# Performance work log

Hardware: AMD Instinct MI355X
Metric: run time of the kernel (lower is better)

Reference implementation:

```python
import jax, jax.numpy as jnp
import numpy as np

EPS = 1e-12  # torch F.normalize eps
NUM_HEADS = 4
DT = 0.25
NUM_STEPS = 4


def _l2norm(x, axis=-1):
    n = jnp.sqrt(jnp.sum(x * x, axis=axis, keepdims=True))
    return x / jnp.maximum(n, EPS)


def setup_inputs() -> dict:
    key = jax.random.key(0)
    k0, k1, k2, k3, k4 = jax.random.split(key, 5)
    B, T, D = 4, 2048, 256
    z = jax.random.normal(k0, (B, T, D), dtype=jnp.float32)
    omega = jax.random.normal(k1, (1, 1, D), dtype=jnp.float32) * 0.1
    Wqk = jax.random.normal(k2, (2 * D, D), dtype=jnp.float32) * (1.0 / np.sqrt(D))
    Wout = jax.random.normal(k3, (D, D), dtype=jnp.float32) * (1.0 / np.sqrt(D))
    bout = jax.random.normal(k4, (D,), dtype=jnp.float32) * 0.01
    return {"z": z, "omega": omega, "Wqk": Wqk, "Wout": Wout, "bout": bout}


def _kuramoto(x, omega, Wqk, Wout, bout):
    # x: [B, T, D]
    B, T, D = x.shape
    hd = D // NUM_HEADS
    qk = x @ Wqk.T  # [B, T, 2D]
    q, k = jnp.split(qk, 2, axis=-1)
    q = _l2norm(q.reshape(B, T, NUM_HEADS, hd))  # cosine-normalized per head
    k = _l2norm(k.reshape(B, T, NUM_HEADS, hd))
    # coupling: [B, H, T, T] cosine similarity
    coupling = jnp.einsum("bqhd,bkhd->bhqk", q, k)
    # sin nonlinearity replaces softmax
    force = jnp.einsum("bhqk,bkhd->bqhd", jnp.sin(coupling), k).reshape(B, T, D)
    return omega + force @ Wout.T + bout


def reference(z, omega, Wqk, Wout, bout):
    def f(x):
        return _kuramoto(x, omega, Wqk, Wout, bout)

    x = z
    for _ in range(NUM_STEPS):
        x = _l2norm(x)
        k1 = f(x)
        k2 = f(x + DT / 2 * k1)
        k3 = f(x + DT / 2 * k2)
        k4 = f(x + DT * k3)
        x = x + DT / 6 * (k1 + 2 * k2 + 2 * k3 + k4)
    return _l2norm(x)
```

## Files before the change

kernel.cpp:

```cpp
#include <hip/hip_runtime.h>
#include <cmath>

#define NB 4
#define TT 2048
#define DD 256
#define NH 4
#define BT (NB*TT)

static constexpr float DT_ = 0.25f;

typedef _Float16 f16x8 __attribute__((ext_vector_type(8)));
typedef _Float16 f16x4 __attribute__((ext_vector_type(4)));
typedef float    f32x4 __attribute__((ext_vector_type(4)));

static constexpr size_t HSZ = (size_t)NB * NH * TT * 64;
static constexpr size_t FSZ = (size_t)BT * 256;

__global__ __launch_bounds__(256)
void split_weights(const float* __restrict__ Wqk, const float* __restrict__ Wout,
                   _Float16* __restrict__ WqkH, _Float16* __restrict__ WqkL,
                   _Float16* __restrict__ WoutH, _Float16* __restrict__ WoutL)
{
    const int idx = blockIdx.x * 256 + threadIdx.x;
    const float4 v = (idx < 32768) ? ((const float4*)Wqk)[idx]
                                   : ((const float4*)Wout)[idx - 32768];
    f16x4 h, l;
    h[0]=(_Float16)v.x; l[0]=(_Float16)(v.x-(float)h[0]);
    h[1]=(_Float16)v.y; l[1]=(_Float16)(v.y-(float)h[1]);
    h[2]=(_Float16)v.z; l[2]=(_Float16)(v.z-(float)h[2]);
    h[3]=(_Float16)v.w; l[3]=(_Float16)(v.w-(float)h[3]);
    if (idx < 32768) { ((f16x4*)WqkH)[idx] = h; ((f16x4*)WqkL)[idx] = l; }
    else { ((f16x4*)WoutH)[idx-32768] = h; ((f16x4*)WoutL)[idx-32768] = l; }
}

__global__ __launch_bounds__(256)
void comb_weights(const float* __restrict__ Wqk, const float* __restrict__ Wout,
                  const float* __restrict__ omega, const float* __restrict__ bout,
                  _Float16* __restrict__ WcombH, _Float16* __restrict__ WcombL,
                  float* __restrict__ qkob)
{
    __shared__ float qrow[256];
    __shared__ float pr[256];
    const int n = blockIdx.x;
    const int k = threadIdx.x;
    qrow[k] = Wqk[n * 256 + k];
    __syncthreads();
    float s = 0.f;
    for (int m = 0; m < 256; ++m) s = fmaf(qrow[m], Wout[m * 256 + k], s);
    const _Float16 h = (_Float16)s;
    WcombH[n * 256 + k] = h;
    WcombL[n * 256 + k] = (_Float16)(s - (float)h);
    pr[k] = (omega[k] + bout[k]) * qrow[k];
    __syncthreads();
    if (k == 0) {
        float t = 0.f;
        for (int i = 0; i < 256; ++i) t += pr[i];
        qkob[n] = t;
    }
}

__global__ __launch_bounds__(256)
void l2norm_rows(const float* __restrict__ src, float* __restrict__ dst,
                 _Float16* __restrict__ dstH, _Float16* __restrict__ dstL) {
    const int wave = threadIdx.x >> 6;
    const int lane = threadIdx.x & 63;
    const size_t row = (size_t)blockIdx.x * 4 + wave;
    float4 v = ((const float4*)(src + row * DD))[lane];
    float ss = v.x*v.x + v.y*v.y + v.z*v.z + v.w*v.w;
    #pragma unroll
    for (int off = 32; off; off >>= 1) ss += __shfl_xor(ss, off, 64);
    const float inv = 1.0f / fmaxf(sqrtf(ss), 1e-12f);
    v.x *= inv; v.y *= inv; v.z *= inv; v.w *= inv;
    ((float4*)(dst + row * DD))[lane] = v;
    if (dstH != nullptr) {
        f16x4 h, l;
        h[0]=(_Float16)v.x; l[0]=(_Float16)(v.x-(float)h[0]);
        h[1]=(_Float16)v.y; l[1]=(_Float16)(v.y-(float)h[1]);
        h[2]=(_Float16)v.z; l[2]=(_Float16)(v.z-(float)h[2]);
        h[3]=(_Float16)v.w; l[3]=(_Float16)(v.w-(float)h[3]);
        ((f16x4*)(dstH + row * DD))[lane] = h;
        ((f16x4*)(dstL + row * DD))[lane] = l;
    }
}

__global__ __launch_bounds__(256)
void gemm_mfma(const _Float16* __restrict__ AH, const _Float16* __restrict__ AL,
               const float* __restrict__ Fp, float* __restrict__ Facc,
               const _Float16* __restrict__ BH, const _Float16* __restrict__ BL,
               float* __restrict__ qkx, const float* __restrict__ qkob,
               const float* __restrict__ omega, const float* __restrict__ bout,
               const float* __restrict__ xin, float* __restrict__ xout,
               _Float16* __restrict__ Qhi, _Float16* __restrict__ Qlo,
               _Float16* __restrict__ Khi, _Float16* __restrict__ Klo,
               _Float16* __restrict__ KtrH,
               int mode, float cc, int faccm)
{
    __shared__ _Float16 Ah[128 * 72];
    __shared__ _Float16 Al[128 * 72];
    __shared__ _Float16 Bh[64 * 72];
    __shared__ _Float16 Bl[64 * 72];
    const int m0 = blockIdx.x * 128, n0 = blockIdx.y * 64;
    const int t  = threadIdx.x;
    const int w  = t >> 6;
    const int l  = t & 63;
    const int lr = l & 15;
    const int lq = l >> 4;

    f32x4 acc[2][4];
    #pragma unroll
    for (int s = 0; s < 2; ++s)
        #pragma unroll
        for (int nt = 0; nt < 4; ++nt) acc[s][nt] = (f32x4){0.f,0.f,0.f,0.f};

    for (int kc = 0; kc < 4; ++kc) {
        const int k0 = kc * 64;
        __syncthreads();
        if (mode == 0) {
            #pragma unroll
            for (int s2 = 0; s2 < 4; ++s2) {
                const int idx = t + 256 * s2;
                const int r = idx >> 3, c8 = (idx & 7) * 8;
                *(uint4*)&Ah[r * 72 + c8] = *(const uint4*)(AH + (size_t)(m0 + r) * 256 + k0 + c8);
                *(uint4*)&Al[r * 72 + c8] = *(const uint4*)(AL + (size_t)(m0 + r) * 256 + k0 + c8);
            }
        } else {
            #pragma unroll
            for (int s2 = 0; s2 < 4; ++s2) {
                const int idx = t + 256 * s2;
                const int r = idx >> 3, c8 = (idx & 7) * 8;
                const size_t go = (size_t)(m0 + r) * 256 + k0 + c8;
                float sv[8] = {0,0,0,0,0,0,0,0};
                if (mode == 2) {
                    const float4 a0 = *(const float4*)(Facc + go);
                    const float4 a1 = *(const float4*)(Facc + go + 4);
                    sv[0]=a0.x; sv[1]=a0.y; sv[2]=a0.z; sv[3]=a0.w;
                    sv[4]=a1.x; sv[5]=a1.y; sv[6]=a1.z; sv[7]=a1.w;
                }
                #pragma unroll
                for (int p = 0; p < 3; ++p) {
                    const float4 a0 = *(const float4*)(Fp + p*FSZ + go);
                    const float4 a1 = *(const float4*)(Fp + p*FSZ + go + 4);
                    sv[0]+=a0.x; sv[1]+=a0.y; sv[2]+=a0.z; sv[3]+=a0.w;
                    sv[4]+=a1.x; sv[5]+=a1.y; sv[6]+=a1.z; sv[7]+=a1.w;
                }
                if (mode == 1 && blockIdx.y == 0) {
                    if (faccm == 1) {
                        *(float4*)(Facc + go)     = make_float4(sv[0], sv[1], sv[2], sv[3]);
                        *(float4*)(Facc + go + 4) = make_float4(sv[4], sv[5], sv[6], sv[7]);
                    } else {
                        float4 f0 = *(const float4*)(Facc + go);
                        float4 f1 = *(const float4*)(Facc + go + 4);
                        f0.x += 2.f*sv[0]; f0.y += 2.f*sv[1]; f0.z += 2.f*sv[2]; f0.w += 2.f*sv[3];
                        f1.x += 2.f*sv[4]; f1.y += 2.f*sv[5]; f1.z += 2.f*sv[6]; f1.w += 2.f*sv[7];
                        *(float4*)(Facc + go)     = f0;
                        *(float4*)(Facc + go + 4) = f1;
                    }
                }
                f16x8 hv, lv;
                #pragma unroll
                for (int e = 0; e < 8; ++e) {
                    hv[e] = (_Float16)sv[e];
                    lv[e] = (_Float16)(sv[e] - (float)hv[e]);
                }
                *(f16x8*)&Ah[r * 72 + c8] = hv;
                *(f16x8*)&Al[r * 72 + c8] = lv;
            }
        }
        #pragma unroll
        for (int s2 = 0; s2 < 2; ++s2) {
            const int idx = t + 256 * s2;
            const int r = idx >> 3, c8 = (idx & 7) * 8;
            *(uint4*)&Bh[r * 72 + c8] = *(const uint4*)(BH + (size_t)(n0 + r) * 256 + k0 + c8);
            *(uint4*)&Bl[r * 72 + c8] = *(const uint4*)(BL + (size_t)(n0 + r) * 256 + k0 + c8);
        }
        __syncthreads();
        #pragma unroll
        for (int c = 0; c < 2; ++c) {
            f16x8 ah[2], al[2], bh[4], bl[4];
            #pragma unroll
            for (int s = 0; s < 2; ++s) {
                ah[s] = *(const f16x8*)&Ah[(32*w + 16*s + lr) * 72 + 32*c + 8*lq];
                al[s] = *(const f16x8*)&Al[(32*w + 16*s + lr) * 72 + 32*c + 8*lq];
            }
            #pragma unroll
            for (int nt = 0; nt < 4; ++nt) {
                bh[nt] = *(const f16x8*)&Bh[(16*nt + lr) * 72 + 32*c + 8*lq];
                bl[nt] = *(const f16x8*)&Bl[(16*nt + lr) * 72 + 32*c + 8*lq];
            }
            #pragma unroll
            for (int s = 0; s < 2; ++s)
                #pragma unroll
                for (int nt = 0; nt < 4; ++nt) {
                    acc[s][nt] = __builtin_amdgcn_mfma_f32_16x16x32_f16(ah[s], bh[nt], acc[s][nt], 0, 0, 0);
                    acc[s][nt] = __builtin_amdgcn_mfma_f32_16x16x32_f16(ah[s], bl[nt], acc[s][nt], 0, 0, 0);
                    acc[s][nt] = __builtin_amdgcn_mfma_f32_16x16x32_f16(al[s], bh[nt], acc[s][nt], 0, 0, 0);
                }
        }
    }

    if (mode == 2) {
        #pragma unroll
        for (int s = 0; s < 2; ++s) {
            const int row0 = m0 + 32*w + 16*s + 4*lq;
            #pragma unroll
            for (int nt = 0; nt < 4; ++nt) {
                const int col = n0 + 16*nt + lr;
                const float ob = omega[col] + bout[col];
                #pragma unroll
                for (int r = 0; r < 4; ++r) {
                    const size_t off = (size_t)(row0 + r) * 256 + col;
                    xout[off] = xin[off] + (DT_ / 6.0f) * acc[s][nt][r] + DT_ * ob;
                }
            }
        }
    } else {
        float val[2][4][4];
        #pragma unroll
        for (int s = 0; s < 2; ++s) {
            const int row0 = m0 + 32*w + 16*s + 4*lq;
            #pragma unroll
            for (int nt = 0; nt < 4; ++nt) {
                const int col = n0 + 16*nt + lr;
                #pragma unroll
                for (int r = 0; r < 4; ++r) {
                    const size_t qo = (size_t)(row0 + r) * 512 + col;
                    if (mode == 0) {
                        val[s][nt][r] = acc[s][nt][r];
                        qkx[qo] = acc[s][nt][r];
                    } else {
                        val[s][nt][r] = qkx[qo] + cc * (acc[s][nt][r] + qkob[col]);
                    }
                }
            }
        }
        float ss[2][4];
        #pragma unroll
        for (int s = 0; s < 2; ++s)
            #pragma unroll
            for (int r = 0; r < 4; ++r) {
                float v = 0.f;
                #pragma unroll
                for (int nt = 0; nt < 4; ++nt) v += val[s][nt][r] * val[s][nt][r];
                ss[s][r] = v;
            }
        #pragma unroll
        for (int off = 1; off < 16; off <<= 1)
            #pragma unroll
            for (int s = 0; s < 2; ++s)
                #pragma unroll
                for (int r = 0; r < 4; ++r)
                    ss[s][r] += __shfl_xor(ss[s][r], off, 64);
        const int  b    = m0 >> 11;
        const int  h    = (n0 >> 6) & 3;
        const bool is_k = (n0 >= 256);
        const size_t bhi = (size_t)b * NH + h;
        _Float16* dhi = (is_k ? Khi : Qhi) + bhi * (size_t)TT * 64;
        _Float16* dlo = (is_k ? Klo : Qlo) + bhi * (size_t)TT * 64;
        const int mloc = m0 & (TT - 1);
        #pragma unroll
        for (int s = 0; s < 2; ++s) {
            const int r0 = 32*w + 16*s + 4*lq;
            float inv[4];
            #pragma unroll
            for (int r = 0; r < 4; ++r) inv[r] = 1.0f / fmaxf(sqrtf(ss[s][r]), 1e-12f);
            #pragma unroll
            for (int nt = 0; nt < 4; ++nt) {
                const int d = 16*nt + lr;
                f16x4 hv, lv;
                #pragma unroll
                for (int r = 0; r < 4; ++r) {
                    const float v2 = val[s][nt][r] * inv[r];
                    hv[r] = (_Float16)v2;
                    lv[r] = (_Float16)(v2 - (float)hv[r]);
                    dhi[(size_t)(mloc + r0 + r) * 64 + d] = hv[r];
                    dlo[(size_t)(mloc + r0 + r) * 64 + d] = lv[r];
                }
                if (is_k) {
                    const size_t tb = bhi * (size_t)64 * TT + (size_t)d * TT + mloc + r0;
                    *(f16x4*)(KtrH + tb) = hv;
                }
            }
        }
    }
}

__global__ __launch_bounds__(256, 3)
void kuramoto_attn(const _Float16* __restrict__ Qhi, const _Float16* __restrict__ Qlo,
                   const _Float16* __restrict__ Khi, const _Float16* __restrict__ Klo,
                   const _Float16* __restrict__ KtrH,
                   float* __restrict__ Fp)
{
    __shared__ _Float16 KjH[64 * 72];
    __shared__ _Float16 KjL[64 * 72];
    __shared__ _Float16 KdH[64 * 72];
    __shared__ _Float16 Pw[4][2][16 * 68];
    const int bh = blockIdx.z;
    const int b  = bh >> 2, h = bh & 3;
    const size_t base  = (size_t)bh * TT * 64;
    const size_t tbase = (size_t)bh * 64 * TT;
    const int t0 = blockIdx.y * 11;
    const int tn = (blockIdx.y == 2) ? 10 : 11;
    float* Fout = Fp + (size_t)blockIdx.y * FSZ;
    const int t = threadIdx.x;
    const int w = t >> 6;
    const int l = t & 63;
    const int lr = l & 15;
    const int lq = l >> 4;
    const int i0 = blockIdx.x * 128 + w * 32;

    f16x8 qh[2][2], ql[2][2];
    #pragma unroll
    for (int s = 0; s < 2; ++s) {
        const size_t qoff = base + (size_t)(i0 + 16*s + lr) * 64 + lq * 8;
        qh[s][0] = *(const f16x8*)(Qhi + qoff);
        qh[s][1] = *(const f16x8*)(Qhi + qoff + 32);
        ql[s][0] = *(const f16x8*)(Qlo + qoff);
        ql[s][1] = *(const f16x8*)(Qlo + qoff + 32);
    }

    f32x4 Facc[2][4];
    #pragma unroll
    for (int s = 0; s < 2; ++s)
        #pragma unroll
        for (int nt = 0; nt < 4; ++nt) Facc[s][nt] = (f32x4){0.f, 0.f, 0.f, 0.f};

    const int sr = t >> 3;
    const int so = (t & 7) * 8;

    for (int tt = 0; tt < tn; ++tt) {
        const int j0 = (t0 + tt) * 64;
        __syncthreads();
        {
            *(uint4*)&KjH[sr * 72 + so]        = *(const uint4*)(Khi + base + (size_t)(j0 + sr) * 64 + so);
            *(uint4*)&KjH[(sr + 32) * 72 + so] = *(const uint4*)(Khi + base + (size_t)(j0 + sr + 32) * 64 + so);
            *(uint4*)&KjL[sr * 72 + so]        = *(const uint4*)(Klo + base + (size_t)(j0 + sr) * 64 + so);
            *(uint4*)&KjL[(sr + 32) * 72 + so] = *(const uint4*)(Klo + base + (size_t)(j0 + sr + 32) * 64 + so);
            *(uint4*)&KdH[sr * 72 + so]        = *(const uint4*)(KtrH + tbase + (size_t)sr * TT + j0 + so);
            *(uint4*)&KdH[(sr + 32) * 72 + so] = *(const uint4*)(KtrH + tbase + (size_t)(sr + 32) * TT + j0 + so);
        }
        __syncthreads();
        #pragma unroll
        for (int nt = 0; nt < 4; ++nt) {
            f16x8 kh0 = *(const f16x8*)&KjH[(16*nt + lr) * 72 + lq * 8];
            f16x8 kh1 = *(const f16x8*)&KjH[(16*nt + lr) * 72 + 32 + lq * 8];
            f16x8 kl0 = *(const f16x8*)&KjL[(16*nt + lr) * 72 + lq * 8];
            f16x8 kl1 = *(const f16x8*)&KjL[(16*nt + lr) * 72 + 32 + lq * 8];
            #pragma unroll
            for (int s = 0; s < 2; ++s) {
                f32x4 a = (f32x4){0.f, 0.f, 0.f, 0.f};
                a = __builtin_amdgcn_mfma_f32_16x16x32_f16(kh0, qh[s][0], a, 0, 0, 0);
                a = __builtin_amdgcn_mfma_f32_16x16x32_f16(kh1, qh[s][1], a, 0, 0, 0);
                a = __builtin_amdgcn_mfma_f32_16x16x32_f16(kl0, qh[s][0], a, 0, 0, 0);
                a = __builtin_amdgcn_mfma_f32_16x16x32_f16(kl1, qh[s][1], a, 0, 0, 0);
                a = __builtin_amdgcn_mfma_f32_16x16x32_f16(kh0, ql[s][0], a, 0, 0, 0);
                a = __builtin_amdgcn_mfma_f32_16x16x32_f16(kh1, ql[s][1], a, 0, 0, 0);
                f16x4 pv;
                #pragma unroll
                for (int r = 0; r < 4; ++r) pv[r] = (_Float16)__sinf(a[r]);
                *(f16x4*)&Pw[w][s][lr * 68 + 16*nt + 4*lq] = pv;
            }
        }
        f16x8 ph[2][2];
        #pragma unroll
        for (int s = 0; s < 2; ++s) {
            ph[s][0] = *(const f16x8*)&Pw[w][s][lr * 68 + lq * 8];
            ph[s][1] = *(const f16x8*)&Pw[w][s][lr * 68 + 32 + lq * 8];
        }
        #pragma unroll
        for (int nt = 0; nt < 4; ++nt) {
            f16x8 kh0 = *(const f16x8*)&KdH[(16*nt + lr) * 72 + lq * 8];
            f16x8 kh1 = *(const f16x8*)&KdH[(16*nt + lr) * 72 + 32 + lq * 8];
            #pragma unroll
            for (int s = 0; s < 2; ++s) {
                Facc[s][nt] = __builtin_amdgcn_mfma_f32_16x16x32_f16(ph[s][0], kh0, Facc[s][nt], 0, 0, 0);
                Facc[s][nt] = __builtin_amdgcn_mfma_f32_16x16x32_f16(ph[s][1], kh1, Facc[s][nt], 0, 0, 0);
            }
        }
    }
    #pragma unroll
    for (int s = 0; s < 2; ++s) {
        float* fo = Fout + ((size_t)b * TT + i0 + 16*s + 4*lq) * 256 + h * 64 + lr;
        #pragma unroll
        for (int nt = 0; nt < 4; ++nt)
            #pragma unroll
            for (int r = 0; r < 4; ++r)
                fo[(size_t)r * 256 + nt * 16] = Facc[s][nt][r];
    }
}

extern "C" void kernel_launch(void* const* d_in, const int* in_sizes, int n_in,
                              void* d_out, int out_size, void* d_ws, size_t ws_size,
                              hipStream_t stream) {
    const float* z     = (const float*)d_in[0];
    const float* omega = (const float*)d_in[1];
    const float* Wqk   = (const float*)d_in[2];
    const float* Wout  = (const float*)d_in[3];
    const float* bout  = (const float*)d_in[4];

    float* x    = (float*)d_ws;
    float* Facc = x + FSZ;
    float* Fp   = Facc + FSZ;
    float* qkx  = Fp + 3 * FSZ;
    float* qkob = qkx + (size_t)BT * 512;
    _Float16* xsH  = (_Float16*)(qkob + 512);
    _Float16* xsL  = xsH  + FSZ;
    _Float16* Qhi  = xsL  + FSZ;
    _Float16* Qlo  = Qhi  + HSZ;
    _Float16* Khi  = Qlo  + HSZ;
    _Float16* Klo  = Khi  + HSZ;
    _Float16* KtrH = Klo  + HSZ;
    _Float16* WqkH = KtrH + HSZ;
    _Float16* WqkL = WqkH + (size_t)512 * 256;
    _Float16* WoutH= WqkL + (size_t)512 * 256;
    _Float16* WoutL= WoutH + (size_t)256 * 256;
    _Float16* WcombH = WoutL + (size_t)256 * 256;
    _Float16* WcombL = WcombH + (size_t)512 * 256;

    split_weights<<<192, 256, 0, stream>>>(Wqk, Wout, WqkH, WqkL, WoutH, WoutL);
    comb_weights<<<512, 256, 0, stream>>>(Wqk, Wout, omega, bout, WcombH, WcombL, qkob);

    for (int step = 0; step < 4; ++step) {
        l2norm_rows<<<BT / 4, 256, 0, stream>>>(step == 0 ? z : x, x, xsH, xsL);
        gemm_mfma<<<dim3(BT / 128, 8), 256, 0, stream>>>(
            xsH, xsL, nullptr, nullptr, WqkH, WqkL, qkx, nullptr,
            nullptr, nullptr, nullptr, nullptr,
            Qhi, Qlo, Khi, Klo, KtrH, 0, 0.f, 0);
        kuramoto_attn<<<dim3(TT / 128, 3, NB * NH), 256, 0, stream>>>(
            Qhi, Qlo, Khi, Klo, KtrH, Fp);
        for (int s = 1; s <= 3; ++s) {
            const float cs = (s == 3) ? 0.25f : 0.125f;
            gemm_mfma<<<dim3(BT / 128, 8), 256, 0, stream>>>(
                nullptr, nullptr, Fp, Facc, WcombH, WcombL, qkx, qkob,
                nullptr, nullptr, nullptr, nullptr,
                Qhi, Qlo, Khi, Klo, KtrH, 1, cs, (s == 1) ? 1 : 2);
            kuramoto_attn<<<dim3(TT / 128, 3, NB * NH), 256, 0, stream>>>(
                Qhi, Qlo, Khi, Klo, KtrH, Fp);
        }
        gemm_mfma<<<dim3(BT / 128, 4), 256, 0, stream>>>(
            nullptr, nullptr, Fp, Facc, WoutH, WoutL, nullptr, nullptr,
            omega, bout, x, x,
            nullptr, nullptr, nullptr, nullptr, nullptr, 2, 0.f, 0);
    }
    l2norm_rows<<<BT / 4, 256, 0, stream>>>(x, (float*)d_out, nullptr, nullptr);
}
```

Before: 1.227 ms.

## Split partial-force reduction into separate kernel and XOR-swizzle LDS tiles

The three-way partial-sum reduction of the attention force and the hi/lo fp16 split move out of the GEMM A-load into a new reduce_F kernel. The GEMM then always loads pre-split fp16 operands, so the 8 column blocks no longer each re-read and re-reduce the fp32 partials. LDS tiles in the GEMM and attention kernels drop the 72-element padding in favor of an XOR swizzle on 64-wide rows, and the GEMM gets a launch-bounds occupancy hint. This costs an extra kernel launch plus an fp16 write and read round trip per stage.

```diff
diff --git a/kernel.cpp b/kernel.cpp
--- a/kernel.cpp
+++ b/kernel.cpp
@@ -84,8 +84,35 @@
 }
 
 __global__ __launch_bounds__(256)
+void reduce_F(const float* __restrict__ Fp, float* __restrict__ Facc,
+              _Float16* __restrict__ SH, _Float16* __restrict__ SL, int faccm)
+{
+    const size_t idx = (size_t)blockIdx.x * 256 + threadIdx.x;
+    const float4 a = ((const float4*)Fp)[idx];
+    const float4 b = ((const float4*)(Fp + FSZ))[idx];
+    const float4 c = ((const float4*)(Fp + 2*FSZ))[idx];
+    float4 s = make_float4(a.x+b.x+c.x, a.y+b.y+c.y, a.z+b.z+c.z, a.w+b.w+c.w);
+    if (faccm == 1) {
+        ((float4*)Facc)[idx] = s;
+    } else if (faccm == 2) {
+        float4 f = ((const float4*)Facc)[idx];
+        f.x += 2.f*s.x; f.y += 2.f*s.y; f.z += 2.f*s.z; f.w += 2.f*s.w;
+        ((float4*)Facc)[idx] = f;
+    } else {
+        const float4 f = ((const float4*)Facc)[idx];
+        s.x += f.x; s.y += f.y; s.z += f.z; s.w += f.w;
+    }
+    f16x4 h, l;
+    h[0]=(_Float16)s.x; l[0]=(_Float16)(s.x-(float)h[0]);
+    h[1]=(_Float16)s.y; l[1]=(_Float16)(s.y-(float)h[1]);
+    h[2]=(_Float16)s.z; l[2]=(_Float16)(s.z-(float)h[2]);
+    h[3]=(_Float16)s.w; l[3]=(_Float16)(s.w-(float)h[3]);
+    ((f16x4*)SH)[idx] = h;
+    ((f16x4*)SL)[idx] = l;
+}
+
+__global__ __launch_bounds__(256, 3)
 void gemm_mfma(const _Float16* __restrict__ AH, const _Float16* __restrict__ AL,
-               const float* __restrict__ Fp, float* __restrict__ Facc,
                const _Float16* __restrict__ BH, const _Float16* __restrict__ BL,
                float* __restrict__ qkx, const float* __restrict__ qkob,
                const float* __restrict__ omega, const float* __restrict__ bout,
@@ -93,12 +120,12 @@
                _Float16* __restrict__ Qhi, _Float16* __restrict__ Qlo,
                _Float16* __restrict__ Khi, _Float16* __restrict__ Klo,
                _Float16* __restrict__ KtrH,
-               int mode, float cc, int faccm)
+               int mode, float cc)
 {
-    __shared__ _Float16 Ah[128 * 72];
-    __shared__ _Float16 Al[128 * 72];
-    __shared__ _Float16 Bh[64 * 72];
-    __shared__ _Float16 Bl[64 * 72];
+    __shared__ _Float16 Ah[128 * 64];
+    __shared__ _Float16 Al[128 * 64];
+    __shared__ _Float16 Bh[64 * 64];
+    __shared__ _Float16 Bl[64 * 64];
     const int m0 = blockIdx.x * 128, n0 = blockIdx.y * 64;
     const int t  = threadIdx.x;
     const int w  = t >> 6;
@@ -112,80 +139,43 @@
         #pragma unroll
         for (int nt = 0; nt < 4; ++nt) acc[s][nt] = (f32x4){0.f,0.f,0.f,0.f};
 
+    int rdo[8];
+    #pragma unroll
+    for (int ch = 0; ch < 8; ++ch) rdo[ch] = ((ch ^ (lr & 7)) * 8);
+
     for (int kc = 0; kc < 4; ++kc) {
         const int k0 = kc * 64;
         __syncthreads();
-        if (mode == 0) {
-            #pragma unroll
-            for (int s2 = 0; s2 < 4; ++s2) {
-                const int idx = t + 256 * s2;
-                const int r = idx >> 3, c8 = (idx & 7) * 8;
-                *(uint4*)&Ah[r * 72 + c8] = *(const uint4*)(AH + (size_t)(m0 + r) * 256 + k0 + c8);
-                *(uint4*)&Al[r * 72 + c8] = *(const uint4*)(AL + (size_t)(m0 + r) * 256 + k0 + c8);
-            }
-        } else {
-            #pragma unroll
-            for (int s2 = 0; s2 < 4; ++s2) {
-                const int idx = t + 256 * s2;
-                const int r = idx >> 3, c8 = (idx & 7) * 8;
-                const size_t go = (size_t)(m0 + r) * 256 + k0 + c8;
-                float sv[8] = {0,0,0,0,0,0,0,0};
-                if (mode == 2) {
-                    const float4 a0 = *(const float4*)(Facc + go);
-                    const float4 a1 = *(const float4*)(Facc + go + 4);
-                    sv[0]=a0.x; sv[1]=a0.y; sv[2]=a0.z; sv[3]=a0.w;
-                    sv[4]=a1.x; sv[5]=a1.y; sv[6]=a1.z; sv[7]=a1.w;
-                }
-                #pragma unroll
-                for (int p = 0; p < 3; ++p) {
-                    const float4 a0 = *(const float4*)(Fp + p*FSZ + go);
-                    const float4 a1 = *(const float4*)(Fp + p*FSZ + go + 4);
-                    sv[0]+=a0.x; sv[1]+=a0.y; sv[2]+=a0.z; sv[3]+=a0.w;
-                    sv[4]+=a1.x; sv[5]+=a1.y; sv[6]+=a1.z; sv[7]+=a1.w;
-                }
-                if (mode == 1 && blockIdx.y == 0) {
-                    if (faccm == 1) {
-                        *(float4*)(Facc + go)     = make_float4(sv[0], sv[1], sv[2], sv[3]);
-                        *(float4*)(Facc + go + 4) = make_float4(sv[4], sv[5], sv[6], sv[7]);
-                    } else {
-                        float4 f0 = *(const float4*)(Facc + go);
-                        float4 f1 = *(const float4*)(Facc + go + 4);
-                        f0.x += 2.f*sv[0]; f0.y += 2.f*sv[1]; f0.z += 2.f*sv[2]; f0.w += 2.f*sv[3];
-                        f1.x += 2.f*sv[4]; f1.y += 2.f*sv[5]; f1.z += 2.f*sv[6]; f1.w += 2.f*sv[7];
-                        *(float4*)(Facc + go)     = f0;
-                        *(float4*)(Facc + go + 4) = f1;
-                    }
-                }
-                f16x8 hv, lv;
-                #pragma unroll
-                for (int e = 0; e < 8; ++e) {
-                    hv[e] = (_Float16)sv[e];
-                    lv[e] = (_Float16)(sv[e] - (float)hv[e]);
-                }
-                *(f16x8*)&Ah[r * 72 + c8] = hv;
-                *(f16x8*)&Al[r * 72 + c8] = lv;
-            }
+        #pragma unroll
+        for (int s2 = 0; s2 < 4; ++s2) {
+            const int idx = t + 256 * s2;
+            const int r = idx >> 3, lc = idx & 7;
+            const int sw = ((lc ^ (r & 7)) * 8);
+            *(uint4*)&Ah[r * 64 + sw] = *(const uint4*)(AH + (size_t)(m0 + r) * 256 + k0 + lc * 8);
+            *(uint4*)&Al[r * 64 + sw] = *(const uint4*)(AL + (size_t)(m0 + r) * 256 + k0 + lc * 8);
         }
         #pragma unroll
         for (int s2 = 0; s2 < 2; ++s2) {
             const int idx = t + 256 * s2;
-            const int r = idx >> 3, c8 = (idx & 7) * 8;
-            *(uint4*)&Bh[r * 72 + c8] = *(const uint4*)(BH + (size_t)(n0 + r) * 256 + k0 + c8);
-            *(uint4*)&Bl[r * 72 + c8] = *(const uint4*)(BL + (size_t)(n0 + r) * 256 + k0 + c8);
+            const int r = idx >> 3, lc = idx & 7;
+            const int sw = ((lc ^ (r & 7)) * 8);
+            *(uint4*)&Bh[r * 64 + sw] = *(const uint4*)(BH + (size_t)(n0 + r) * 256 + k0 + lc * 8);
+            *(uint4*)&Bl[r * 64 + sw] = *(const uint4*)(BL + (size_t)(n0 + r) * 256 + k0 + lc * 8);
         }
         __syncthreads();
         #pragma unroll
         for (int c = 0; c < 2; ++c) {
+            const int xo = rdo[4*c + lq];
             f16x8 ah[2], al[2], bh[4], bl[4];
             #pragma unroll
             for (int s = 0; s < 2; ++s) {
-                ah[s] = *(const f16x8*)&Ah[(32*w + 16*s + lr) * 72 + 32*c + 8*lq];
-                al[s] = *(const f16x8*)&Al[(32*w + 16*s + lr) * 72 + 32*c + 8*lq];
+                ah[s] = *(const f16x8*)&Ah[(32*w + 16*s + lr) * 64 + xo];
+                al[s] = *(const f16x8*)&Al[(32*w + 16*s + lr) * 64 + xo];
             }
             #pragma unroll
             for (int nt = 0; nt < 4; ++nt) {
-                bh[nt] = *(const f16x8*)&Bh[(16*nt + lr) * 72 + 32*c + 8*lq];
-                bl[nt] = *(const f16x8*)&Bl[(16*nt + lr) * 72 + 32*c + 8*lq];
+                bh[nt] = *(const f16x8*)&Bh[(16*nt + lr) * 64 + xo];
+                bl[nt] = *(const f16x8*)&Bl[(16*nt + lr) * 64 + xo];
             }
             #pragma unroll
             for (int s = 0; s < 2; ++s)
@@ -290,9 +280,9 @@
                    const _Float16* __restrict__ KtrH,
                    float* __restrict__ Fp)
 {
-    __shared__ _Float16 KjH[64 * 72];
-    __shared__ _Float16 KjL[64 * 72];
-    __shared__ _Float16 KdH[64 * 72];
+    __shared__ _Float16 KjH[64 * 64];
+    __shared__ _Float16 KjL[64 * 64];
+    __shared__ _Float16 KdH[64 * 64];
     __shared__ _Float16 Pw[4][2][16 * 68];
     const int bh = blockIdx.z;
     const int b  = bh >> 2, h = bh & 3;
@@ -325,26 +315,30 @@
         for (int nt = 0; nt < 4; ++nt) Facc[s][nt] = (f32x4){0.f, 0.f, 0.f, 0.f};
 
     const int sr = t >> 3;
-    const int so = (t & 7) * 8;
+    const int lc = t & 7;
+    const int so = lc * 8;
+    const int sw = ((lc ^ (sr & 7)) * 8);
+    const int x0 = ((lq     ^ (lr & 7)) * 8);
+    const int x1 = (((lq+4) ^ (lr & 7)) * 8);
 
     for (int tt = 0; tt < tn; ++tt) {
         const int j0 = (t0 + tt) * 64;
         __syncthreads();
         {
-            *(uint4*)&KjH[sr * 72 + so]        = *(const uint4*)(Khi + base + (size_t)(j0 + sr) * 64 + so);
-            *(uint4*)&KjH[(sr + 32) * 72 + so] = *(const uint4*)(Khi + base + (size_t)(j0 + sr + 32) * 64 + so);
-            *(uint4*)&KjL[sr * 72 + so]        = *(const uint4*)(Klo + base + (size_t)(j0 + sr) * 64 + so);
-            *(uint4*)&KjL[(sr + 32) * 72 + so] = *(const uint4*)(Klo + base + (size_t)(j0 + sr + 32) * 64 + so);
-            *(uint4*)&KdH[sr * 72 + so]        = *(const uint4*)(KtrH + tbase + (size_t)sr * TT + j0 + so);
-            *(uint4*)&KdH[(sr + 32) * 72 + so] = *(const uint4*)(KtrH + tbase + (size_t)(sr + 32) * TT + j0 + so);
+            *(uint4*)&KjH[sr * 64 + sw]        = *(const uint4*)(Khi + base + (size_t)(j0 + sr) * 64 + so);
+            *(uint4*)&KjH[(sr + 32) * 64 + sw] = *(const uint4*)(Khi + base + (size_t)(j0 + sr + 32) * 64 + so);
+            *(uint4*)&KjL[sr * 64 + sw]        = *(const uint4*)(Klo + base + (size_t)(j0 + sr) * 64 + so);
+            *(uint4*)&KjL[(sr + 32) * 64 + sw] = *(const uint4*)(Klo + base + (size_t)(j0 + sr + 32) * 64 + so);
+            *(uint4*)&KdH[sr * 64 + sw]        = *(const uint4*)(KtrH + tbase + (size_t)sr * TT + j0 + so);
+            *(uint4*)&KdH[(sr + 32) * 64 + sw] = *(const uint4*)(KtrH + tbase + (size_t)(sr + 32) * TT + j0 + so);
         }
         __syncthreads();
         #pragma unroll
         for (int nt = 0; nt < 4; ++nt) {
-            f16x8 kh0 = *(const f16x8*)&KjH[(16*nt + lr) * 72 + lq * 8];
-            f16x8 kh1 = *(const f16x8*)&KjH[(16*nt + lr) * 72 + 32 + lq * 8];
-            f16x8 kl0 = *(const f16x8*)&KjL[(16*nt + lr) * 72 + lq * 8];
-            f16x8 kl1 = *(const f16x8*)&KjL[(16*nt + lr) * 72 + 32 + lq * 8];
+            f16x8 kh0 = *(const f16x8*)&KjH[(16*nt + lr) * 64 + x0];
+            f16x8 kh1 = *(const f16x8*)&KjH[(16*nt + lr) * 64 + x1];
+            f16x8 kl0 = *(const f16x8*)&KjL[(16*nt + lr) * 64 + x0];
+            f16x8 kl1 = *(const f16x8*)&KjL[(16*nt + lr) * 64 + x1];
             #pragma unroll
             for (int s = 0; s < 2; ++s) {
                 f32x4 a = (f32x4){0.f, 0.f, 0.f, 0.f};
@@ -368,8 +362,8 @@
         }
         #pragma unroll
         for (int nt = 0; nt < 4; ++nt) {
-            f16x8 kh0 = *(const f16x8*)&KdH[(16*nt + lr) * 72 + lq * 8];
-            f16x8 kh1 = *(const f16x8*)&KdH[(16*nt + lr) * 72 + 32 + lq * 8];
+            f16x8 kh0 = *(const f16x8*)&KdH[(16*nt + lr) * 64 + x0];
+            f16x8 kh1 = *(const f16x8*)&KdH[(16*nt + lr) * 64 + x1];
             #pragma unroll
             for (int s = 0; s < 2; ++s) {
                 Facc[s][nt] = __builtin_amdgcn_mfma_f32_16x16x32_f16(ph[s][0], kh0, Facc[s][nt], 0, 0, 0);
@@ -422,24 +416,26 @@
     for (int step = 0; step < 4; ++step) {
         l2norm_rows<<<BT / 4, 256, 0, stream>>>(step == 0 ? z : x, x, xsH, xsL);
         gemm_mfma<<<dim3(BT / 128, 8), 256, 0, stream>>>(
-            xsH, xsL, nullptr, nullptr, WqkH, WqkL, qkx, nullptr,
+            xsH, xsL, WqkH, WqkL, qkx, nullptr,
             nullptr, nullptr, nullptr, nullptr,
-            Qhi, Qlo, Khi, Klo, KtrH, 0, 0.f, 0);
+            Qhi, Qlo, Khi, Klo, KtrH, 0, 0.f);
         kuramoto_attn<<<dim3(TT / 128, 3, NB * NH), 256, 0, stream>>>(
             Qhi, Qlo, Khi, Klo, KtrH, Fp);
         for (int s = 1; s <= 3; ++s) {
             const float cs = (s == 3) ? 0.25f : 0.125f;
+            reduce_F<<<2048, 256, 0, stream>>>(Fp, Facc, xsH, xsL, (s == 1) ? 1 : 2);
             gemm_mfma<<<dim3(BT / 128, 8), 256, 0, stream>>>(
-                nullptr, nullptr, Fp, Facc, WcombH, WcombL, qkx, qkob,
+                xsH, xsL, WcombH, WcombL, qkx, qkob,
                 nullptr, nullptr, nullptr, nullptr,
-                Qhi, Qlo, Khi, Klo, KtrH, 1, cs, (s == 1) ? 1 : 2);
+                Qhi, Qlo, Khi, Klo, KtrH, 1, cs);
             kuramoto_attn<<<dim3(TT / 128, 3, NB * NH), 256, 0, stream>>>(
                 Qhi, Qlo, Khi, Klo, KtrH, Fp);
         }
+        reduce_F<<<2048, 256, 0, stream>>>(Fp, Facc, xsH, xsL, 3);
         gemm_mfma<<<dim3(BT / 128, 4), 256, 0, stream>>>(
-            nullptr, nullptr, Fp, Facc, WoutH, WoutL, nullptr, nullptr,
+            xsH, xsL, WoutH, WoutL, nullptr, nullptr,
             omega, bout, x, x,
-            nullptr, nullptr, nullptr, nullptr, nullptr, 2, 0.f, 0);
+            nullptr, nullptr, nullptr, nullptr, nullptr, 2, 0.f);
     }
     l2norm_rows<<<BT / 4, 256, 0, stream>>>(x, (float*)d_out, nullptr, nullptr);
 }
```

After: 1.287 ms. +4.8%, slower.
